# Optimization experiments

Hardware: AMD Instinct MI355X
Metric: run time of the kernel (lower is better)

Reference implementation:

```python
import jax, jax.numpy as jnp
import numpy as np

# Hardcoded in FixedActionDecoder.__init__:
# action_words = [[click,submit,target,focus],[select,text,noun,username,password],[copy],[paste]]
ACTION_INDEX = jnp.array([0, 0, 0, 0, 1, 1, 1, 1, 1, 2, 3], dtype=jnp.int32)
POINT_SIZE = 11
ACTION_SIZE = 4
EPS = 1e-8  # F.cosine_similarity default eps


def setup_inputs() -> dict:
    key = jax.random.key(0)
    k1, k2 = jax.random.split(key)
    B, D = 1_000_000, 64
    return {
        "embedded_words": jax.random.normal(k1, (B, D), dtype=jnp.float32),
        "action_vectors": jax.random.normal(k2, (D, POINT_SIZE), dtype=jnp.float32),
    }


def reference(embedded_words, action_vectors):
    # Cosine similarity along the embedding dim (torch clamps each norm to eps).
    x = embedded_words / jnp.maximum(
        jnp.linalg.norm(embedded_words, axis=1, keepdims=True), EPS)          # [B, D]
    a = action_vectors / jnp.maximum(
        jnp.linalg.norm(action_vectors, axis=0, keepdims=True), EPS)          # [D, P]
    sims = x @ a                                                              # [B, P]
    # global_max_pool over batch_action_index == per-batch segment-max over actions.
    seg = jax.ops.segment_max(sims.T, ACTION_INDEX,
                              num_segments=ACTION_SIZE).T                     # [B, A]
    action_idx = jnp.argmax(seg, axis=1)                                      # [B]
    # one-hot scatter: ret[action_idx] = 1.0
    return jax.nn.one_hot(action_idx, ACTION_SIZE, dtype=embedded_words.dtype)
```

## Files before the change

kernel.cpp:

```cpp
#include <hip/hip_runtime.h>


#define NP 11
#define TAU 1e-3f
#define LROW 36

__device__ __align__(16) float g_W32[704];
__device__ double g_W64[704];
__device__ unsigned long long g_bits[1 << 20];

__global__ void prep(const float* __restrict__ A) {
    __shared__ double sq[64][NP + 1];
    __shared__ double sc[NP];
    const int d = threadIdx.x;
    double a[NP];
    #pragma unroll
    for (int p = 0; p < NP; ++p) {
        a[p] = (double)A[d * NP + p];
        sq[d][p] = a[p] * a[p];
    }
    __syncthreads();
    if (d < NP) {
        double ss = 0.0;
        #pragma unroll
        for (int r = 0; r < 64; ++r) ss += sq[r][d];
        sc[d] = 1.0 / fmax(sqrt(ss), 1e-8);
    }
    __syncthreads();
    #pragma unroll
    for (int p = 0; p < NP; ++p) {
        double w = a[p] * sc[p];
        g_W64[d * NP + p] = w;
        g_W32[(d >> 2) * 44 + p * 4 + (d & 3)] = (float)w;
    }
}

__device__ __forceinline__ void argmax_gap(const float* s, int& idx, float& gap) {
    float m0 = fmaxf(fmaxf(s[0], s[1]), fmaxf(s[2], s[3]));
    float m1 = fmaxf(fmaxf(fmaxf(s[4], s[5]), s[6]), fmaxf(s[7], s[8]));
    float m2 = s[9], m3 = s[10];
    idx = 0; float best = m0;
    if (m1 > best) { best = m1; idx = 1; }
    if (m2 > best) { best = m2; idx = 2; }
    if (m3 > best) { best = m3; idx = 3; }
    float second = -3.4e38f;
    if (idx != 0) second = fmaxf(second, m0);
    if (idx != 1) second = fmaxf(second, m1);
    if (idx != 2) second = fmaxf(second, m2);
    if (idx != 3) second = fmaxf(second, m3);
    gap = best - second;
}

__global__ __launch_bounds__(128) void decode(const float* __restrict__ X,
                                              float* __restrict__ out, int B) {
    __shared__ float xbuf[2][128][LROW];
    __shared__ float w_lds[704];

    const int tid = threadIdx.x;
    const int lane = tid & 63;
    const int wv = tid >> 6;
    float(*buf)[LROW] = xbuf[wv];

    for (int t = tid; t < 176; t += 128)
        reinterpret_cast<float4*>(w_lds)[t] =
            reinterpret_cast<const float4*>(g_W32)[t];
    __syncthreads();

    const float4* X4 = reinterpret_cast<const float4*>(X);
    const int gwave = blockIdx.x * 2 + wv;
    const int nwaves = gridDim.x * 2;

    #pragma unroll 1
    for (int base = gwave * 128; base < B; base += nwaves * 128) {
        float acc0[NP], acc1[NP];
        #pragma unroll
        for (int p = 0; p < NP; ++p) { acc0[p] = 0.0f; acc1[p] = 0.0f; }

        #pragma unroll
        for (int st = 0; st < 2; ++st) {
            #pragma unroll
            for (int i = 0; i < 16; ++i) {
                int fid = i * 64 + lane;
                int row = fid >> 3;
                int f = fid & 7;
                int r = base + row;
                if (r >= B) r = B - 1;
                float4 v = X4[(size_t)r * 16 + st * 8 + f];
                *reinterpret_cast<float4*>(&buf[row][f * 4]) = v;
            }
            __builtin_amdgcn_wave_barrier();

            #pragma unroll 1
            for (int kk = 0; kk < 8; ++kk) {
                const float* wrow = &w_lds[(st * 8 + kk) * 44];
                float4 x0 = *reinterpret_cast<const float4*>(&buf[lane][kk * 4]);
                float4 x1 = *reinterpret_cast<const float4*>(&buf[lane + 64][kk * 4]);
                #pragma unroll
                for (int p = 0; p < NP; ++p) {
                    float4 wq = *reinterpret_cast<const float4*>(&wrow[p * 4]);
                    float t0 = fmaf(x0.x, wq.x, acc0[p]);
                    t0 = fmaf(x0.y, wq.y, t0);
                    t0 = fmaf(x0.z, wq.z, t0);
                    acc0[p] = fmaf(x0.w, wq.w, t0);
                    float t1 = fmaf(x1.x, wq.x, acc1[p]);
                    t1 = fmaf(x1.y, wq.y, t1);
                    t1 = fmaf(x1.z, wq.z, t1);
                    acc1[p] = fmaf(x1.w, wq.w, t1);
                }
            }
            __builtin_amdgcn_wave_barrier();
        }

        int idx0, idx1; float gap0, gap1;
        argmax_gap(acc0, idx0, gap0);
        argmax_gap(acc1, idx1, gap1);

        unsigned long long m0 = __ballot(gap0 < TAU);
        unsigned long long m1 = __ballot(gap1 < TAU);
        if (lane == 0) {
            g_bits[(base >> 6) + 0] = m0;
            g_bits[(base >> 6) + 1] = m1;
        }

        int r0 = base + lane, r1 = base + 64 + lane;
        if (r0 < B) {
            float4 o;
            o.x = (idx0 == 0) ? 1.0f : 0.0f;
            o.y = (idx0 == 1) ? 1.0f : 0.0f;
            o.z = (idx0 == 2) ? 1.0f : 0.0f;
            o.w = (idx0 == 3) ? 1.0f : 0.0f;
            reinterpret_cast<float4*>(out)[r0] = o;
        }
        if (r1 < B) {
            float4 o;
            o.x = (idx1 == 0) ? 1.0f : 0.0f;
            o.y = (idx1 == 1) ? 1.0f : 0.0f;
            o.z = (idx1 == 2) ? 1.0f : 0.0f;
            o.w = (idx1 == 3) ? 1.0f : 0.0f;
            reinterpret_cast<float4*>(out)[r1] = o;
        }
    }
}

__global__ __launch_bounds__(256) void repair(const float* __restrict__ X,
                                              float* __restrict__ out, int B) {
    __shared__ double w64[704];
    const int tid = threadIdx.x;
    for (int i = tid; i < 704; i += 256) w64[i] = g_W64[i];
    __syncthreads();

    const int nwords = (B + 63) >> 6;
    for (int t = blockIdx.x * blockDim.x + tid; t < nwords;
         t += gridDim.x * blockDim.x) {
        unsigned long long m = g_bits[t];
        while (m) {
            int b = __builtin_ctzll(m);
            m &= m - 1;
            int row = t * 64 + b;
            if (row >= B) continue;

            double s[NP];
            #pragma unroll
            for (int p = 0; p < NP; ++p) s[p] = 0.0;
            #pragma unroll 1
            for (int d = 0; d < 64; ++d) {
                double x = (double)X[(size_t)row * 64 + d];
                #pragma unroll
                for (int p = 0; p < NP; ++p)
                    s[p] = fma(x, w64[d * NP + p], s[p]);
            }

            double m0 = fmax(fmax(s[0], s[1]), fmax(s[2], s[3]));
            double m1 = fmax(fmax(fmax(s[4], s[5]), s[6]), fmax(s[7], s[8]));
            double m2 = s[9], m3 = s[10];
            int idx = 0; double best = m0;
            if (m1 > best) { best = m1; idx = 1; }
            if (m2 > best) { best = m2; idx = 2; }
            if (m3 > best) { best = m3; idx = 3; }

            float4 o;
            o.x = (idx == 0) ? 1.0f : 0.0f;
            o.y = (idx == 1) ? 1.0f : 0.0f;
            o.z = (idx == 2) ? 1.0f : 0.0f;
            o.w = (idx == 3) ? 1.0f : 0.0f;
            reinterpret_cast<float4*>(out)[row] = o;
        }
    }
}

extern "C" void kernel_launch(void* const* d_in, const int* in_sizes, int n_in,
                              void* d_out, int out_size, void* d_ws, size_t ws_size,
                              hipStream_t stream) {
    const float* X = (const float*)d_in[0];
    const float* A = (const float*)d_in[1];
    float* out = (float*)d_out;
    const int B = in_sizes[0] / 64;

    hipLaunchKernelGGL(prep, dim3(1), dim3(64), 0, stream, A);
    hipLaunchKernelGGL(decode, dim3(1024), dim3(128), 0, stream, X, out, B);
    hipLaunchKernelGGL(repair, dim3(128), dim3(256), 0, stream, X, out, B);
}
```

Measured before the change: 78.28 us.

## Double-buffer X tiles via direct global-to-LDS loads and fuse repair inline

X tiles are now loaded with global_load_lds directly into two per-wave LDS buffers with an XOR swizzle. The next tile's loads are issued while the current tile is computed, gated by explicit vmcnt waits. The separate repair kernel and its bitmask buffer are removed: rows with a small top-two gap are recomputed in fp64 inline, inside a wave-uniform branch that should rarely be taken. The grid is halved to 512 blocks and one kernel launch is dropped. The risks are fragile hand-written waitcnt accounting and divergent fp64 work in the hot kernel.

```diff
diff --git a/kernel.cpp b/kernel.cpp
--- a/kernel.cpp
+++ b/kernel.cpp
@@ -3,11 +3,9 @@
 
 #define NP 11
 #define TAU 1e-3f
-#define LROW 36
 
 __device__ __align__(16) float g_W32[704];
 __device__ double g_W64[704];
-__device__ unsigned long long g_bits[1 << 20];
 
 __global__ void prep(const float* __restrict__ A) {
     __shared__ double sq[64][NP + 1];
@@ -34,6 +32,40 @@
         g_W32[(d >> 2) * 44 + p * 4 + (d & 3)] = (float)w;
     }
 }
+
+#define ISSUE(tbase, phase, ldsbuf)                                            \
+    {                                                                          \
+        _Pragma("unroll") for (int i = 0; i < 16; ++i) {                       \
+            int r = (tbase) + i * 8 + hi3;                                     \
+            if (r >= B) r = B - 1;     \
+            const float4* src = X4 + (size_t)r * 16 + (phase) * 8 + fsrc;      \
+            __builtin_amdgcn_global_load_lds(                                  \
+                (const __attribute__((address_space(1))) void*)src,            \
+                (__attribute__((address_space(3))) void*)((ldsbuf) + i * 64),  \
+                16, 0, 0);                                                     \
+        }                                                                      \
+    }
+
+#define COMPUTE(phase, bufp)                                                   \
+    {                                                                          \
+        _Pragma("unroll 1") for (int kk = 0; kk < 8; ++kk) {                   \
+            const int sw = kk ^ s7;                                            \
+            float4 x0 = (bufp)[lane * 8 + sw];                                 \
+            float4 x1 = (bufp)[(lane + 64) * 8 + sw];                          \
+            const float* wrow = &w_lds[((phase) * 8 + kk) * 44];               \
+            _Pragma("unroll") for (int p = 0; p < NP; ++p) {                   \
+                float4 wq = *reinterpret_cast<const float4*>(&wrow[p * 4]);    \
+                float t0 = fmaf(x0.x, wq.x, acc0[p]);                          \
+                t0 = fmaf(x0.y, wq.y, t0);                                     \
+                t0 = fmaf(x0.z, wq.z, t0);                                     \
+                acc0[p] = fmaf(x0.w, wq.w, t0);                                \
+                float t1 = fmaf(x1.x, wq.x, acc1[p]);                          \
+                t1 = fmaf(x1.y, wq.y, t1);                                     \
+                t1 = fmaf(x1.z, wq.z, t1);                                     \
+                acc1[p] = fmaf(x1.w, wq.w, t1);                                \
+            }                                                                  \
+        }                                                                      \
+    }
 
 __device__ __forceinline__ void argmax_gap(const float* s, int& idx, float& gap) {
     float m0 = fmaxf(fmaxf(s[0], s[1]), fmaxf(s[2], s[3]));
@@ -51,78 +83,89 @@
     gap = best - second;
 }
 
+__device__ int repair_row(const float* __restrict__ X, int row) {
+    double s[NP];
+    #pragma unroll
+    for (int p = 0; p < NP; ++p) s[p] = 0.0;
+    #pragma unroll 1
+    for (int d = 0; d < 64; ++d) {
+        double x = (double)X[(size_t)row * 64 + d];
+        #pragma unroll
+        for (int p = 0; p < NP; ++p)
+            s[p] = fma(x, g_W64[d * NP + p], s[p]);
+    }
+    double m0 = fmax(fmax(s[0], s[1]), fmax(s[2], s[3]));
+    double m1 = fmax(fmax(fmax(s[4], s[5]), s[6]), fmax(s[7], s[8]));
+    double m2 = s[9], m3 = s[10];
+    int idx = 0; double best = m0;
+    if (m1 > best) { best = m1; idx = 1; }
+    if (m2 > best) { best = m2; idx = 2; }
+    if (m3 > best) { best = m3; idx = 3; }
+    return idx;
+}
+
 __global__ __launch_bounds__(128) void decode(const float* __restrict__ X,
                                               float* __restrict__ out, int B) {
-    __shared__ float xbuf[2][128][LROW];
+    __shared__ float4 sbuf[2][2][1024];
     __shared__ float w_lds[704];
 
     const int tid = threadIdx.x;
     const int lane = tid & 63;
     const int wv = tid >> 6;
-    float(*buf)[LROW] = xbuf[wv];
+    const int s7 = lane & 7;
+    const int hi3 = lane >> 3;
+    const int fsrc = s7 ^ hi3;
 
     for (int t = tid; t < 176; t += 128)
         reinterpret_cast<float4*>(w_lds)[t] =
             reinterpret_cast<const float4*>(g_W32)[t];
     __syncthreads();
 
+    float4* bufA = &sbuf[wv][0][0];
+    float4* bufB = &sbuf[wv][1][0];
     const float4* X4 = reinterpret_cast<const float4*>(X);
     const int gwave = blockIdx.x * 2 + wv;
-    const int nwaves = gridDim.x * 2;
+    const int stride = gridDim.x * 2 * 128;
+    const int base0 = gwave * 128;
+    if (base0 >= B) return;
+
+    ISSUE(base0, 0, bufA);
+    ISSUE(base0, 1, bufB);
 
     #pragma unroll 1
-    for (int base = gwave * 128; base < B; base += nwaves * 128) {
+    for (int base = base0; base < B; base += stride) {
+        const int next = base + stride;
+        const bool pf = next < B;
+
         float acc0[NP], acc1[NP];
         #pragma unroll
         for (int p = 0; p < NP; ++p) { acc0[p] = 0.0f; acc1[p] = 0.0f; }
 
-        #pragma unroll
-        for (int st = 0; st < 2; ++st) {
-            #pragma unroll
-            for (int i = 0; i < 16; ++i) {
-                int fid = i * 64 + lane;
-                int row = fid >> 3;
-                int f = fid & 7;
-                int r = base + row;
-                if (r >= B) r = B - 1;
-                float4 v = X4[(size_t)r * 16 + st * 8 + f];
-                *reinterpret_cast<float4*>(&buf[row][f * 4]) = v;
-            }
-            __builtin_amdgcn_wave_barrier();
-
-            #pragma unroll 1
-            for (int kk = 0; kk < 8; ++kk) {
-                const float* wrow = &w_lds[(st * 8 + kk) * 44];
-                float4 x0 = *reinterpret_cast<const float4*>(&buf[lane][kk * 4]);
-                float4 x1 = *reinterpret_cast<const float4*>(&buf[lane + 64][kk * 4]);
-                #pragma unroll
-                for (int p = 0; p < NP; ++p) {
-                    float4 wq = *reinterpret_cast<const float4*>(&wrow[p * 4]);
-                    float t0 = fmaf(x0.x, wq.x, acc0[p]);
-                    t0 = fmaf(x0.y, wq.y, t0);
-                    t0 = fmaf(x0.z, wq.z, t0);
-                    acc0[p] = fmaf(x0.w, wq.w, t0);
-                    float t1 = fmaf(x1.x, wq.x, acc1[p]);
-                    t1 = fmaf(x1.y, wq.y, t1);
-                    t1 = fmaf(x1.z, wq.z, t1);
-                    acc1[p] = fmaf(x1.w, wq.w, t1);
-                }
-            }
-            __builtin_amdgcn_wave_barrier();
-        }
+        asm volatile("s_waitcnt vmcnt(16)" ::: "memory");
+        __builtin_amdgcn_sched_barrier(0);
+        COMPUTE(0, bufA);
+        if (pf) ISSUE(next, 0, bufA);
+
+        if (pf) {
+            asm volatile("s_waitcnt vmcnt(16)" ::: "memory");
+        } else {
+            asm volatile("s_waitcnt vmcnt(0)" ::: "memory");
+        }
+        __builtin_amdgcn_sched_barrier(0);
+        COMPUTE(1, bufB);
 
         int idx0, idx1; float gap0, gap1;
         argmax_gap(acc0, idx0, gap0);
         argmax_gap(acc1, idx1, gap1);
 
-        unsigned long long m0 = __ballot(gap0 < TAU);
-        unsigned long long m1 = __ballot(gap1 < TAU);
-        if (lane == 0) {
-            g_bits[(base >> 6) + 0] = m0;
-            g_bits[(base >> 6) + 1] = m1;
-        }
-
-        int r0 = base + lane, r1 = base + 64 + lane;
+        const int r0 = base + lane, r1 = base + 64 + lane;
+        const bool f0 = (gap0 < TAU) && (r0 < B);
+        const bool f1 = (gap1 < TAU) && (r1 < B);
+        if (__builtin_expect(__any(f0 || f1), 0)) {
+            if (f0) idx0 = repair_row(X, r0);
+            if (f1) idx1 = repair_row(X, r1);
+        }
+
         if (r0 < B) {
             float4 o;
             o.x = (idx0 == 0) ? 1.0f : 0.0f;
@@ -139,52 +182,8 @@
             o.w = (idx1 == 3) ? 1.0f : 0.0f;
             reinterpret_cast<float4*>(out)[r1] = o;
         }
-    }
-}
-
-__global__ __launch_bounds__(256) void repair(const float* __restrict__ X,
-                                              float* __restrict__ out, int B) {
-    __shared__ double w64[704];
-    const int tid = threadIdx.x;
-    for (int i = tid; i < 704; i += 256) w64[i] = g_W64[i];
-    __syncthreads();
-
-    const int nwords = (B + 63) >> 6;
-    for (int t = blockIdx.x * blockDim.x + tid; t < nwords;
-         t += gridDim.x * blockDim.x) {
-        unsigned long long m = g_bits[t];
-        while (m) {
-            int b = __builtin_ctzll(m);
-            m &= m - 1;
-            int row = t * 64 + b;
-            if (row >= B) continue;
-
-            double s[NP];
-            #pragma unroll
-            for (int p = 0; p < NP; ++p) s[p] = 0.0;
-            #pragma unroll 1
-            for (int d = 0; d < 64; ++d) {
-                double x = (double)X[(size_t)row * 64 + d];
-                #pragma unroll
-                for (int p = 0; p < NP; ++p)
-                    s[p] = fma(x, w64[d * NP + p], s[p]);
-            }
-
-            double m0 = fmax(fmax(s[0], s[1]), fmax(s[2], s[3]));
-            double m1 = fmax(fmax(fmax(s[4], s[5]), s[6]), fmax(s[7], s[8]));
-            double m2 = s[9], m3 = s[10];
-            int idx = 0; double best = m0;
-            if (m1 > best) { best = m1; idx = 1; }
-            if (m2 > best) { best = m2; idx = 2; }
-            if (m3 > best) { best = m3; idx = 3; }
-
-            float4 o;
-            o.x = (idx == 0) ? 1.0f : 0.0f;
-            o.y = (idx == 1) ? 1.0f : 0.0f;
-            o.z = (idx == 2) ? 1.0f : 0.0f;
-            o.w = (idx == 3) ? 1.0f : 0.0f;
-            reinterpret_cast<float4*>(out)[row] = o;
-        }
+
+        if (pf) ISSUE(next, 1, bufB);
     }
 }
 
@@ -197,6 +196,5 @@
     const int B = in_sizes[0] / 64;
 
     hipLaunchKernelGGL(prep, dim3(1), dim3(64), 0, stream, A);
-    hipLaunchKernelGGL(decode, dim3(1024), dim3(128), 0, stream, X, out, B);
-    hipLaunchKernelGGL(repair, dim3(128), dim3(256), 0, stream, X, out, B);
-}
+    hipLaunchKernelGGL(decode, dim3(512), dim3(128), 0, stream, X, out, B);
+}
```

Measured after the change: 124.9 us. 1.6x slower.

## Fuse near-tie fp64 repair into decode kernel and drop separate repair pass

Applied to the files above, without the earlier changes.

Rows whose top-two segment scores are within the tolerance are now recomputed in double precision inline in the decode kernel, behind a wave-level any() branch, via a noinline helper that reads fp64 weights from global memory. This removes the third kernel launch, the bitmask writes to global memory and the repair kernel's full scan over the bitmask words. In exchange, waves that hit a near-tie stall while one or two lanes do a serial 64-step fp64 dot product, and the noinline call may add register or spill overhead to the decode kernel.

```diff
diff --git a/kernel.cpp b/kernel.cpp
--- a/kernel.cpp
+++ b/kernel.cpp
@@ -7,7 +7,6 @@
 
 __device__ __align__(16) float g_W32[704];
 __device__ double g_W64[704];
-__device__ unsigned long long g_bits[1 << 20];
 
 __global__ void prep(const float* __restrict__ A) {
     __shared__ double sq[64][NP + 1];
@@ -49,6 +48,27 @@
     if (idx != 2) second = fmaxf(second, m2);
     if (idx != 3) second = fmaxf(second, m3);
     gap = best - second;
+}
+
+__device__ __noinline__ int repair_row(const float* __restrict__ X, int row) {
+    double s[NP];
+    #pragma unroll
+    for (int p = 0; p < NP; ++p) s[p] = 0.0;
+    #pragma unroll 1
+    for (int d = 0; d < 64; ++d) {
+        double x = (double)X[(size_t)row * 64 + d];
+        #pragma unroll
+        for (int p = 0; p < NP; ++p)
+            s[p] = fma(x, g_W64[d * NP + p], s[p]);
+    }
+    double m0 = fmax(fmax(s[0], s[1]), fmax(s[2], s[3]));
+    double m1 = fmax(fmax(fmax(s[4], s[5]), s[6]), fmax(s[7], s[8]));
+    double m2 = s[9], m3 = s[10];
+    int idx = 0; double best = m0;
+    if (m1 > best) { best = m1; idx = 1; }
+    if (m2 > best) { best = m2; idx = 2; }
+    if (m3 > best) { best = m3; idx = 3; }
+    return idx;
 }
 
 __global__ __launch_bounds__(128) void decode(const float* __restrict__ X,
@@ -115,14 +135,14 @@
         argmax_gap(acc0, idx0, gap0);
         argmax_gap(acc1, idx1, gap1);
 
-        unsigned long long m0 = __ballot(gap0 < TAU);
-        unsigned long long m1 = __ballot(gap1 < TAU);
-        if (lane == 0) {
-            g_bits[(base >> 6) + 0] = m0;
-            g_bits[(base >> 6) + 1] = m1;
+        const int r0 = base + lane, r1 = base + 64 + lane;
+        const bool f0 = (gap0 < TAU) && (r0 < B);
+        const bool f1 = (gap1 < TAU) && (r1 < B);
+        if (__builtin_expect(__any(f0 || f1), 0)) {
+            if (f0) idx0 = repair_row(X, r0);
+            if (f1) idx1 = repair_row(X, r1);
         }
 
-        int r0 = base + lane, r1 = base + 64 + lane;
         if (r0 < B) {
             float4 o;
             o.x = (idx0 == 0) ? 1.0f : 0.0f;
@@ -142,52 +162,6 @@
     }
 }
 
-__global__ __launch_bounds__(256) void repair(const float* __restrict__ X,
-                                              float* __restrict__ out, int B) {
-    __shared__ double w64[704];
-    const int tid = threadIdx.x;
-    for (int i = tid; i < 704; i += 256) w64[i] = g_W64[i];
-    __syncthreads();
-
-    const int nwords = (B + 63) >> 6;
-    for (int t = blockIdx.x * blockDim.x + tid; t < nwords;
-         t += gridDim.x * blockDim.x) {
-        unsigned long long m = g_bits[t];
-        while (m) {
-            int b = __builtin_ctzll(m);
-            m &= m - 1;
-            int row = t * 64 + b;
-            if (row >= B) continue;
-
-            double s[NP];
-            #pragma unroll
-            for (int p = 0; p < NP; ++p) s[p] = 0.0;
-            #pragma unroll 1
-            for (int d = 0; d < 64; ++d) {
-                double x = (double)X[(size_t)row * 64 + d];
-                #pragma unroll
-                for (int p = 0; p < NP; ++p)
-                    s[p] = fma(x, w64[d * NP + p], s[p]);
-            }
-
-            double m0 = fmax(fmax(s[0], s[1]), fmax(s[2], s[3]));
-            double m1 = fmax(fmax(fmax(s[4], s[5]), s[6]), fmax(s[7], s[8]));
-            double m2 = s[9], m3 = s[10];
-            int idx = 0; double best = m0;
-            if (m1 > best) { best = m1; idx = 1; }
-            if (m2 > best) { best = m2; idx = 2; }
-            if (m3 > best) { best = m3; idx = 3; }
-
-            float4 o;
-            o.x = (idx == 0) ? 1.0f : 0.0f;
-            o.y = (idx == 1) ? 1.0f : 0.0f;
-            o.z = (idx == 2) ? 1.0f : 0.0f;
-            o.w = (idx == 3) ? 1.0f : 0.0f;
-            reinterpret_cast<float4*>(out)[row] = o;
-        }
-    }
-}
-
 extern "C" void kernel_launch(void* const* d_in, const int* in_sizes, int n_in,
                               void* d_out, int out_size, void* d_ws, size_t ws_size,
                               hipStream_t stream) {
@@ -198,5 +172,4 @@
 
     hipLaunchKernelGGL(prep, dim3(1), dim3(64), 0, stream, A);
     hipLaunchKernelGGL(decode, dim3(1024), dim3(128), 0, stream, X, out, B);
-    hipLaunchKernelGGL(repair, dim3(128), dim3(256), 0, stream, X, out, B);
 }
```

New measurement: 98.73 us. +26.1%, slower.

## Load rows directly from global per lane, drop LDS staging, double block size

Applied to the files above, without the earlier changes.

The decode kernel no longer stages X tiles through shared memory with coalesced loads. Each lane now reads its own row straight from global memory, one float4 at a time, across 16 k-steps. Blocks grow from 2 to 4 waves, which doubles the number of resident waves doing the streaming. This removes the LDS write/read traffic and wave barriers, but the per-lane row reads are strided by 256 bytes across lanes, so access is uncoalesced and relies on cache-line reuse across the k iterations.

```diff
diff --git a/kernel.cpp b/kernel.cpp
--- a/kernel.cpp
+++ b/kernel.cpp
@@ -3,7 +3,6 @@
 
 #define NP 11
 #define TAU 1e-3f
-#define LROW 36
 
 __device__ __align__(16) float g_W32[704];
 __device__ double g_W64[704];
@@ -51,64 +50,53 @@
     gap = best - second;
 }
 
-__global__ __launch_bounds__(128) void decode(const float* __restrict__ X,
+__global__ __launch_bounds__(256) void decode(const float* __restrict__ X,
                                               float* __restrict__ out, int B) {
-    __shared__ float xbuf[2][128][LROW];
     __shared__ float w_lds[704];
 
     const int tid = threadIdx.x;
     const int lane = tid & 63;
     const int wv = tid >> 6;
-    float(*buf)[LROW] = xbuf[wv];
 
-    for (int t = tid; t < 176; t += 128)
+    for (int t = tid; t < 176; t += 256)
         reinterpret_cast<float4*>(w_lds)[t] =
             reinterpret_cast<const float4*>(g_W32)[t];
     __syncthreads();
 
     const float4* X4 = reinterpret_cast<const float4*>(X);
-    const int gwave = blockIdx.x * 2 + wv;
-    const int nwaves = gridDim.x * 2;
+    const int gwave = blockIdx.x * 4 + wv;
+    const int nwaves = gridDim.x * 4;
 
     #pragma unroll 1
     for (int base = gwave * 128; base < B; base += nwaves * 128) {
+        const int r0 = base + lane;
+        const int r1 = base + 64 + lane;
+        const int cr0 = (r0 < B) ? r0 : (B - 1);
+        const int cr1 = (r1 < B) ? r1 : (B - 1);
+        const float4* __restrict__ row0 = X4 + (size_t)cr0 * 16;
+        const float4* __restrict__ row1 = X4 + (size_t)cr1 * 16;
+
         float acc0[NP], acc1[NP];
         #pragma unroll
         for (int p = 0; p < NP; ++p) { acc0[p] = 0.0f; acc1[p] = 0.0f; }
 
-        #pragma unroll
-        for (int st = 0; st < 2; ++st) {
+        #pragma unroll 2
+        for (int kk = 0; kk < 16; ++kk) {
+            float4 x0 = row0[kk];
+            float4 x1 = row1[kk];
+            const float* wrow = &w_lds[kk * 44];
             #pragma unroll
-            for (int i = 0; i < 16; ++i) {
-                int fid = i * 64 + lane;
-                int row = fid >> 3;
-                int f = fid & 7;
-                int r = base + row;
-                if (r >= B) r = B - 1;
-                float4 v = X4[(size_t)r * 16 + st * 8 + f];
-                *reinterpret_cast<float4*>(&buf[row][f * 4]) = v;
+            for (int p = 0; p < NP; ++p) {
+                float4 wq = *reinterpret_cast<const float4*>(&wrow[p * 4]);
+                float t0 = fmaf(x0.x, wq.x, acc0[p]);
+                t0 = fmaf(x0.y, wq.y, t0);
+                t0 = fmaf(x0.z, wq.z, t0);
+                acc0[p] = fmaf(x0.w, wq.w, t0);
+                float t1 = fmaf(x1.x, wq.x, acc1[p]);
+                t1 = fmaf(x1.y, wq.y, t1);
+                t1 = fmaf(x1.z, wq.z, t1);
+                acc1[p] = fmaf(x1.w, wq.w, t1);
             }
-            __builtin_amdgcn_wave_barrier();
-
-            #pragma unroll 1
-            for (int kk = 0; kk < 8; ++kk) {
-                const float* wrow = &w_lds[(st * 8 + kk) * 44];
-                float4 x0 = *reinterpret_cast<const float4*>(&buf[lane][kk * 4]);
-                float4 x1 = *reinterpret_cast<const float4*>(&buf[lane + 64][kk * 4]);
-                #pragma unroll
-                for (int p = 0; p < NP; ++p) {
-                    float4 wq = *reinterpret_cast<const float4*>(&wrow[p * 4]);
-                    float t0 = fmaf(x0.x, wq.x, acc0[p]);
-                    t0 = fmaf(x0.y, wq.y, t0);
-                    t0 = fmaf(x0.z, wq.z, t0);
-                    acc0[p] = fmaf(x0.w, wq.w, t0);
-                    float t1 = fmaf(x1.x, wq.x, acc1[p]);
-                    t1 = fmaf(x1.y, wq.y, t1);
-                    t1 = fmaf(x1.z, wq.z, t1);
-                    acc1[p] = fmaf(x1.w, wq.w, t1);
-                }
-            }
-            __builtin_amdgcn_wave_barrier();
         }
 
         int idx0, idx1; float gap0, gap1;
@@ -122,7 +110,6 @@
             g_bits[(base >> 6) + 1] = m1;
         }
 
-        int r0 = base + lane, r1 = base + 64 + lane;
         if (r0 < B) {
             float4 o;
             o.x = (idx0 == 0) ? 1.0f : 0.0f;
@@ -197,6 +184,6 @@
     const int B = in_sizes[0] / 64;
 
     hipLaunchKernelGGL(prep, dim3(1), dim3(64), 0, stream, A);
-    hipLaunchKernelGGL(decode, dim3(1024), dim3(128), 0, stream, X, out, B);
+    hipLaunchKernelGGL(decode, dim3(1024), dim3(256), 0, stream, X, out, B);
     hipLaunchKernelGGL(repair, dim3(128), dim3(256), 0, stream, X, out, B);
 }
```

Result: slower. 213.6 us (+172.9%).
